# Kernel optimization log

Hardware: AMD Instinct MI355X
Metric: run time of the kernel (lower is better)

The kernel has to match this reference:

```python
import jax, jax.numpy as jnp
import numpy as np

D = 1024
H = 16
DH = D // H  # 64
B, S = 4, 1024


def setup_inputs() -> dict:
    key = jax.random.key(0)
    ks = jax.random.split(key, 7)
    sequences = jax.random.normal(ks[0], (B, S, D), dtype=jnp.float32)
    scale = 1.0 / np.sqrt(DH)
    Wq = jax.random.normal(ks[1], (H, DH, DH), dtype=jnp.float32) * scale
    Wk = jax.random.normal(ks[2], (H, DH, DH), dtype=jnp.float32) * scale
    Wv = jax.random.normal(ks[3], (H, DH, DH), dtype=jnp.float32) * scale
    bq = jax.random.normal(ks[4], (H, DH), dtype=jnp.float32) * 0.01
    bk = jax.random.normal(ks[5], (H, DH), dtype=jnp.float32) * 0.01
    bv = jax.random.normal(ks[6], (H, DH), dtype=jnp.float32) * 0.01
    return {"sequences": sequences, "Wq": Wq, "Wk": Wk, "Wv": Wv,
            "bq": bq, "bk": bk, "bv": bv}


def reference(sequences, Wq, Wk, Wv, bq, bk, bv):
    b, s, d = sequences.shape
    x = sequences.reshape(b, s, H, DH)  # split channels into heads
    # per-head Linear: y = x @ W.T + b (torch convention)
    q = jnp.einsum('bshd,hed->bshe', x, Wq) + bq
    k = jnp.einsum('bshd,hed->bshe', x, Wk) + bk
    v = jnp.einsum('bshd,hed->bshe', x, Wv) + bv
    inv_sqrt_dh = jnp.asarray(1.0 / np.sqrt(DH), dtype=sequences.dtype)
    scores = jnp.einsum('bshe,bthe->bhst', q, k) * inv_sqrt_dh  # [B,H,S,S]
    attn = jax.nn.softmax(scores, axis=-1)
    out = jnp.einsum('bhst,bthe->bshe', attn, v)  # [B,S,H,DH]
    return out.reshape(b, s, d)  # hstack of heads == reshape here
```

## Files before the change

kernel.cpp:

```cpp
#include <hip/hip_runtime.h>

#define H 16
#define DH 64
#define BB 4
#define SS 1024
#define DD 1024

typedef __attribute__((ext_vector_type(8))) short bf16x8;
typedef __attribute__((ext_vector_type(4))) float f32x4;
typedef __attribute__((ext_vector_type(4))) unsigned int u32x4;
typedef __attribute__((ext_vector_type(2))) unsigned int u32x2;
typedef _Float16 f16x4 __attribute__((ext_vector_type(4)));
typedef _Float16 f16x8 __attribute__((ext_vector_type(8)));
typedef __fp16 hf16x2 __attribute__((ext_vector_type(2)));

#define QSCALE 0.18033688011112042f

#if __has_builtin(__builtin_amdgcn_exp2f)
__device__ __forceinline__ float fast_exp2(float x) {
    return __builtin_amdgcn_exp2f(x);
}
#else
__device__ __forceinline__ float fast_exp2(float x) {
    float r;
    asm("v_exp_f32 %0, %1" : "=v"(r) : "v"(x));
    return r;
}
#endif

__device__ __forceinline__ unsigned short f2bf(float f) {
    union { float f; unsigned u; } v; v.f = f;
    unsigned u = v.u;
    return (unsigned short)((u + 0x7FFFu + ((u >> 16) & 1u)) >> 16);
}

__device__ __forceinline__ unsigned short f2h(float f) {
    union { _Float16 h; unsigned short u; } v;
    v.h = (_Float16)f;
    return v.u;
}

__device__ __forceinline__ void pack8(unsigned short* dst, f32x4 a, f32x4 b) {
    unsigned u0 = (unsigned)f2bf(a[0]) | ((unsigned)f2bf(a[1]) << 16);
    unsigned u1 = (unsigned)f2bf(a[2]) | ((unsigned)f2bf(a[3]) << 16);
    unsigned u2 = (unsigned)f2bf(b[0]) | ((unsigned)f2bf(b[1]) << 16);
    unsigned u3 = (unsigned)f2bf(b[2]) | ((unsigned)f2bf(b[3]) << 16);
    u32x4 v = {u0, u1, u2, u3};
    *(u32x4*)dst = v;
}

__device__ __forceinline__ void async_cp1k(const unsigned short* g,
                                           unsigned short* l, int lane) {
    __builtin_amdgcn_global_load_lds(
        (const __attribute__((address_space(1))) unsigned int*)(g + lane * 8),
        (__attribute__((address_space(3))) unsigned int*)l, 16, 0, 0);
}

__global__ __launch_bounds__(256) void wprep_kernel(
    const float* __restrict__ Wq, const float* __restrict__ Wk,
    const float* __restrict__ Wv, unsigned short* __restrict__ Wp)
{
    const int tg = blockIdx.x * 256 + threadIdx.x;
    const int r = tg >> 2, part = tg & 3;
    const int e = r & 63, hm = r >> 6;
    const int m = hm % 3, h = hm / 3;
    const float* src = (m == 0 ? Wq : (m == 1 ? Wk : Wv)) +
                       (size_t)(h * 64 + e) * 64 + part * 16;
    const float scale = (m == 0) ? QSCALE : 1.0f;
    f32x4 f0 = ((const f32x4*)src)[0];
    f32x4 f1 = ((const f32x4*)src)[1];
    f32x4 f2 = ((const f32x4*)src)[2];
    f32x4 f3 = ((const f32x4*)src)[3];
    f0 *= scale; f1 *= scale; f2 *= scale; f3 *= scale;
    unsigned short tmp[16];
    pack8(tmp, f0, f1);
    pack8(tmp + 8, f2, f3);
    unsigned short* dst = Wp + (size_t)(hm * 64 + e) * 64;
    const int c0 = part * 2, sw = e & 7;
    *(u32x4*)(dst + (c0 ^ sw) * 8)       = *(const u32x4*)tmp;
    *(u32x4*)(dst + ((c0 + 1) ^ sw) * 8) = *(const u32x4*)(tmp + 8);
}

__global__ __launch_bounds__(256) void qkv_kernel(
    const float* __restrict__ x, const unsigned short* __restrict__ Wp,
    const float* __restrict__ bq, const float* __restrict__ bk,
    const float* __restrict__ bv,
    unsigned short* __restrict__ Qg, unsigned short* __restrict__ Kg,
    unsigned short* __restrict__ VTg)
{
    __shared__ __align__(16) unsigned short Xl[4096];
    __shared__ __align__(16) unsigned short Wl[12288];

    const int bid = blockIdx.x;
    const int sc = bid & 15, h = (bid >> 4) & 15, b = bid >> 8;
    const int s0 = sc * 64;
    const int tid = threadIdx.x;
    const int lane = tid & 63, w = tid >> 6;

    {
        const unsigned short* wbase = Wp + (size_t)h * 12288;
#pragma unroll
        for (int sub = 0; sub < 6; sub++) {
            const int off = w * 3072 + sub * 512;
            async_cp1k(wbase + off, &Wl[off], lane);
        }
    }
    {
        const int s = tid >> 2, part = tid & 3;
        const float* src = x + ((size_t)(b * SS + s0 + s)) * DD + h * DH + part * 16;
        f32x4 f0 = ((const f32x4*)src)[0];
        f32x4 f1 = ((const f32x4*)src)[1];
        f32x4 f2 = ((const f32x4*)src)[2];
        f32x4 f3 = ((const f32x4*)src)[3];
        unsigned short tmp[16];
        pack8(tmp, f0, f1);
        pack8(tmp + 8, f2, f3);
        const int c0 = part * 2, sws = s & 7;
        *(u32x4*)&Xl[s * 64 + (c0 ^ sws) * 8]       = *(const u32x4*)tmp;
        *(u32x4*)&Xl[s * 64 + ((c0 + 1) ^ sws) * 8] = *(const u32x4*)(tmp + 8);
    }
    __syncthreads();

    const int l15 = lane & 15, quad = lane >> 4, sw = l15 & 7;

    f32x4 acc[3][4];
#pragma unroll
    for (int m = 0; m < 3; m++)
#pragma unroll
        for (int nt = 0; nt < 4; nt++) acc[m][nt] = (f32x4){0.f, 0.f, 0.f, 0.f};

#pragma unroll
    for (int k2 = 0; k2 < 2; k2++) {
        const int csw = (((k2 << 2) | quad) ^ sw) * 8;
        bf16x8 a = *(const bf16x8*)&Xl[(w * 16 + l15) * 64 + csw];
#pragma unroll
        for (int nt = 0; nt < 4; nt++) {
            const int boff = (nt * 16 + l15) * 64 + csw;
            bf16x8 b0 = *(const bf16x8*)&Wl[boff];
            acc[0][nt] = __builtin_amdgcn_mfma_f32_16x16x32_bf16(a, b0, acc[0][nt], 0, 0, 0);
            bf16x8 b1 = *(const bf16x8*)&Wl[4096 + boff];
            acc[1][nt] = __builtin_amdgcn_mfma_f32_16x16x32_bf16(a, b1, acc[1][nt], 0, 0, 0);
            bf16x8 b2 = *(const bf16x8*)&Wl[8192 + boff];
            acc[2][nt] = __builtin_amdgcn_mfma_f32_16x16x32_bf16(a, b2, acc[2][nt], 0, 0, 0);
        }
    }
    __syncthreads();

#pragma unroll
    for (int nt = 0; nt < 4; nt++) {
        const int e = nt * 16 + l15;
        const float bqs = bq[h * DH + e] * QSCALE;
        const float bks = bk[h * DH + e];
        const float bvs = bv[h * DH + e];
#pragma unroll
        for (int r = 0; r < 4; r++) {
            const int srow = w * 16 + quad * 4 + r;
            Xl[srow * 64 + e] = f2bf(acc[0][nt][r] + bqs);
            Wl[srow * 64 + e] = f2bf(acc[1][nt][r] + bks);
        }
        unsigned v01 = (unsigned)f2h(acc[2][nt][0] + bvs) |
                       ((unsigned)f2h(acc[2][nt][1] + bvs) << 16);
        unsigned v23 = (unsigned)f2h(acc[2][nt][2] + bvs) |
                       ((unsigned)f2h(acc[2][nt][3] + bvs) << 16);
        u32x2 pv = {v01, v23};
        *(u32x2*)&Wl[4096 + w * 1024 + e * 16 + quad * 4] = pv;
    }
    __syncthreads();
    {
        const size_t bh = (size_t)(b * H + h);
        const int row = tid >> 2, part = tid & 3;
        const int cg = part * 16, c0 = part * 2, swr = row & 7;
        unsigned short* qdst = Qg + (bh * SS + s0 + row) * DH + cg;
        *(u32x4*)qdst       = *(const u32x4*)&Xl[row * 64 + cg];
        *(u32x4*)(qdst + 8) = *(const u32x4*)&Xl[row * 64 + cg + 8];
        unsigned short* kbase = Kg + (bh * 16 + sc) * 4096 + row * 64;
        *(u32x4*)(kbase + (c0 ^ swr) * 8)       = *(const u32x4*)&Wl[row * 64 + c0 * 8];
        *(u32x4*)(kbase + ((c0 + 1) ^ swr) * 8) = *(const u32x4*)&Wl[row * 64 + c0 * 8 + 8];
        unsigned short* vdst = VTg + (bh * 16 + sc) * 4096 + tid * 16;
        *(u32x4*)vdst       = *(const u32x4*)&Wl[4096 + tid * 16];
        *(u32x4*)(vdst + 8) = *(const u32x4*)&Wl[4096 + tid * 16 + 8];
    }
}

__global__ __launch_bounds__(256) void attn_kernel(
    const unsigned short* __restrict__ Qg, const unsigned short* __restrict__ Kg,
    const unsigned short* __restrict__ VTg, float* __restrict__ out)
{
    __shared__ __align__(16) unsigned short L[16384];

    const int bid = blockIdx.x;
    const int bh = bid & 63, qt = bid >> 6;
    const int h = bh & 15, b = bh >> 4;
    const int tid = threadIdx.x;
    const int lane = tid & 63, w = tid >> 6;
    const int l15 = lane & 15, quad = lane >> 4, sw = l15 & 7;

    const unsigned short* Kt = Kg + (size_t)bh * 16 * 4096 + w * 1024;
    const unsigned short* Vt = VTg + (size_t)bh * 16 * 4096 + w * 1024;
    unsigned short* Lw = &L[w * 4096];

    const int kb0 = l15 * 64 + ((quad)     ^ sw) * 8;
    const int kb1 = l15 * 64 + ((4 | quad) ^ sw) * 8;
    const int vb  = 1024 + l15 * 16 + quad * 4;

    bf16x8 aQ0[4], aQ1[4];
#pragma unroll
    for (int qb = 0; qb < 4; qb++) {
        const unsigned short* qp =
            Qg + ((size_t)bh * SS + qt * 64 + qb * 16 + l15) * DH + quad * 8;
        aQ0[qb] = *(const bf16x8*)(qp);
        aQ1[qb] = *(const bf16x8*)(qp + 32);
    }

    auto stage = [&](int kt, int bufb) {
        const unsigned short* kg = Kt + kt * 4096;
        const unsigned short* vg = Vt + kt * 4096;
        unsigned short* lb = Lw + bufb * 2048;
        async_cp1k(kg,       lb,        lane);
        async_cp1k(kg + 512, lb + 512,  lane);
        async_cp1k(vg,       lb + 1024, lane);
        async_cp1k(vg + 512, lb + 1536, lane);
    };

    stage(0, 0);
    stage(1, 1);

    f32x4 accO[4][4];
#pragma unroll
    for (int et = 0; et < 4; et++)
#pragma unroll
        for (int qb = 0; qb < 4; qb++) accO[et][qb] = (f32x4){0.f, 0.f, 0.f, 0.f};
    float rs[4] = {0.f, 0.f, 0.f, 0.f};

#pragma unroll
    for (int kt = 0; kt < 16; kt++) {
        if (kt < 15) asm volatile("s_waitcnt vmcnt(4)" ::: "memory");
        else         asm volatile("s_waitcnt vmcnt(0)" ::: "memory");
        const unsigned short* Bc = Lw + (kt & 1) * 2048;

        bf16x8 aK0 = *(const bf16x8*)(Bc + kb0);
        bf16x8 aK1 = *(const bf16x8*)(Bc + kb1);
        f16x4 aV[4];
#pragma unroll
        for (int et = 0; et < 4; et++)
            aV[et] = *(const f16x4*)(Bc + vb + et * 256);
        asm volatile("s_waitcnt lgkmcnt(0)" ::: "memory");
        if (kt < 14) stage(kt + 2, kt & 1);

        f32x4 sc[4];
#pragma unroll
        for (int qb = 0; qb < 4; qb++) {
            f32x4 z = {0.f, 0.f, 0.f, 0.f};
            z = __builtin_amdgcn_mfma_f32_16x16x32_bf16(aK0, aQ0[qb], z, 0, 0, 0);
            z = __builtin_amdgcn_mfma_f32_16x16x32_bf16(aK1, aQ1[qb], z, 0, 0, 0);
            sc[qb] = z;
        }

        f16x4 pf[4];
#pragma unroll
        for (int qb = 0; qb < 4; qb++) {
            float p0 = fast_exp2(sc[qb][0]);
            float p1 = fast_exp2(sc[qb][1]);
            float p2 = fast_exp2(sc[qb][2]);
            float p3 = fast_exp2(sc[qb][3]);
            rs[qb] += (p0 + p1) + (p2 + p3);
            union { hf16x2 h; unsigned u; } lo, hi;
            lo.h = __builtin_amdgcn_cvt_pkrtz(p0, p1);
            hi.h = __builtin_amdgcn_cvt_pkrtz(p2, p3);
            union { unsigned u[2]; f16x4 v; } pk;
            pk.u[0] = lo.u; pk.u[1] = hi.u;
            pf[qb] = pk.v;
        }

#pragma unroll
        for (int et = 0; et < 4; et++) {
#pragma unroll
            for (int qb = 0; qb < 4; qb++)
                accO[et][qb] = __builtin_amdgcn_mfma_f32_16x16x16f16(
                    aV[et], pf[qb], accO[et][qb], 0, 0, 0);
        }
    }

#pragma unroll
    for (int qb = 0; qb < 4; qb++) {
        rs[qb] += __shfl_xor(rs[qb], 16);
        rs[qb] += __shfl_xor(rs[qb], 32);
    }

    __syncthreads();

    float* R  = (float*)L;
    float* R2 = (float*)L + 5120;
    if (quad == 0) {
#pragma unroll
        for (int qb = 0; qb < 4; qb++) R2[w * 64 + qb * 16 + l15] = rs[qb];
    }

    const int q = tid >> 2, eg = tid & 3;
    float inv = 0.f;
#pragma unroll
    for (int et = 0; et < 4; et++) {
#pragma unroll
        for (int qb = 0; qb < 4; qb++)
            *(f32x4*)&R[w * 1280 + (qb * 16 + l15) * 20 + quad * 4] = accO[et][qb];
        __syncthreads();
        if (et == 0)
            inv = 1.0f / (R2[q] + R2[64 + q] + R2[128 + q] + R2[192 + q]);
        f32x4 o0 = *(const f32x4*)&R[q * 20 + eg * 4];
        f32x4 o1 = *(const f32x4*)&R[1280 + q * 20 + eg * 4];
        f32x4 o2 = *(const f32x4*)&R[2560 + q * 20 + eg * 4];
        f32x4 o3 = *(const f32x4*)&R[3840 + q * 20 + eg * 4];
        f32x4 o = ((o0 + o1) + (o2 + o3)) * inv;
        float* op = out + ((size_t)b * SS + qt * 64 + q) * DD + h * DH + et * 16 + eg * 4;
        *(f32x4*)op = o;
        if (et < 3) __syncthreads();
    }
}

extern "C" void kernel_launch(void* const* d_in, const int* in_sizes, int n_in,
                              void* d_out, int out_size, void* d_ws, size_t ws_size,
                              hipStream_t stream) {
    const float* x  = (const float*)d_in[0];
    const float* Wq = (const float*)d_in[1];
    const float* Wk = (const float*)d_in[2];
    const float* Wv = (const float*)d_in[3];
    const float* bq = (const float*)d_in[4];
    const float* bk = (const float*)d_in[5];
    const float* bv = (const float*)d_in[6];

    const size_t NE = (size_t)BB * H * SS * DH;
    unsigned short* Qg  = (unsigned short*)d_ws;
    unsigned short* Kg  = Qg + NE;
    unsigned short* VTg = Kg + NE;
    unsigned short* Wp  = VTg + NE;

    wprep_kernel<<<48, 256, 0, stream>>>(Wq, Wk, Wv, Wp);
    qkv_kernel<<<BB * H * (SS / 64), 256, 0, stream>>>(x, Wp, bq, bk, bv,
                                                       Qg, Kg, VTg);
    attn_kernel<<<BB * H * 16, 256, 0, stream>>>(Qg, Kg, VTg, (float*)d_out);
}
```

Baseline: 116.9 us.

## Fuse weight prep into QKV kernel and stage Q through LDS in attention

Removes the separate weight-prep kernel launch. Each QKV block now converts, scales and swizzles its head's fp32 weights into LDS directly, which repeats that conversion per block. Q is written in the same swizzled tile layout as K. The attention kernel loads Q into LDS asynchronously and reads the fragments per key tile instead of holding them in registers, with a 4-blocks-per-CU launch bound to cut register pressure and raise occupancy. In exchange it adds LDS reads per tile and more LDS use per block.

```diff
diff --git a/kernel.cpp b/kernel.cpp
--- a/kernel.cpp
+++ b/kernel.cpp
@@ -56,33 +56,10 @@
         (__attribute__((address_space(3))) unsigned int*)l, 16, 0, 0);
 }
 
-__global__ __launch_bounds__(256) void wprep_kernel(
+__global__ __launch_bounds__(256) void qkv_kernel(
+    const float* __restrict__ x,
     const float* __restrict__ Wq, const float* __restrict__ Wk,
-    const float* __restrict__ Wv, unsigned short* __restrict__ Wp)
-{
-    const int tg = blockIdx.x * 256 + threadIdx.x;
-    const int r = tg >> 2, part = tg & 3;
-    const int e = r & 63, hm = r >> 6;
-    const int m = hm % 3, h = hm / 3;
-    const float* src = (m == 0 ? Wq : (m == 1 ? Wk : Wv)) +
-                       (size_t)(h * 64 + e) * 64 + part * 16;
-    const float scale = (m == 0) ? QSCALE : 1.0f;
-    f32x4 f0 = ((const f32x4*)src)[0];
-    f32x4 f1 = ((const f32x4*)src)[1];
-    f32x4 f2 = ((const f32x4*)src)[2];
-    f32x4 f3 = ((const f32x4*)src)[3];
-    f0 *= scale; f1 *= scale; f2 *= scale; f3 *= scale;
-    unsigned short tmp[16];
-    pack8(tmp, f0, f1);
-    pack8(tmp + 8, f2, f3);
-    unsigned short* dst = Wp + (size_t)(hm * 64 + e) * 64;
-    const int c0 = part * 2, sw = e & 7;
-    *(u32x4*)(dst + (c0 ^ sw) * 8)       = *(const u32x4*)tmp;
-    *(u32x4*)(dst + ((c0 + 1) ^ sw) * 8) = *(const u32x4*)(tmp + 8);
-}
-
-__global__ __launch_bounds__(256) void qkv_kernel(
-    const float* __restrict__ x, const unsigned short* __restrict__ Wp,
+    const float* __restrict__ Wv,
     const float* __restrict__ bq, const float* __restrict__ bk,
     const float* __restrict__ bv,
     unsigned short* __restrict__ Qg, unsigned short* __restrict__ Kg,
@@ -97,13 +74,26 @@
     const int tid = threadIdx.x;
     const int lane = tid & 63, w = tid >> 6;
 
-    {
-        const unsigned short* wbase = Wp + (size_t)h * 12288;
-#pragma unroll
-        for (int sub = 0; sub < 6; sub++) {
-            const int off = w * 3072 + sub * 512;
-            async_cp1k(wbase + off, &Wl[off], lane);
-        }
+#pragma unroll
+    for (int i = 0; i < 3; i++) {
+        const int task = tid + i * 256;
+        const int r = task >> 2, part = task & 3;
+        const int m = r >> 6, e = r & 63;
+        const float* src = (m == 0 ? Wq : (m == 1 ? Wk : Wv)) +
+                           (size_t)(h * 64 + e) * 64 + part * 16;
+        const float scale = (m == 0) ? QSCALE : 1.0f;
+        f32x4 f0 = ((const f32x4*)src)[0];
+        f32x4 f1 = ((const f32x4*)src)[1];
+        f32x4 f2 = ((const f32x4*)src)[2];
+        f32x4 f3 = ((const f32x4*)src)[3];
+        f0 *= scale; f1 *= scale; f2 *= scale; f3 *= scale;
+        unsigned short tmp[16];
+        pack8(tmp, f0, f1);
+        pack8(tmp + 8, f2, f3);
+        unsigned short* dst = &Wl[m * 4096 + e * 64];
+        const int c0 = part * 2, swe = e & 7;
+        *(u32x4*)(dst + (c0 ^ swe) * 8)       = *(const u32x4*)tmp;
+        *(u32x4*)(dst + ((c0 + 1) ^ swe) * 8) = *(const u32x4*)(tmp + 8);
     }
     {
         const int s = tid >> 2, part = tid & 3;
@@ -169,10 +159,10 @@
     {
         const size_t bh = (size_t)(b * H + h);
         const int row = tid >> 2, part = tid & 3;
-        const int cg = part * 16, c0 = part * 2, swr = row & 7;
-        unsigned short* qdst = Qg + (bh * SS + s0 + row) * DH + cg;
-        *(u32x4*)qdst       = *(const u32x4*)&Xl[row * 64 + cg];
-        *(u32x4*)(qdst + 8) = *(const u32x4*)&Xl[row * 64 + cg + 8];
+        const int c0 = part * 2, swr = row & 7;
+        unsigned short* qbase = Qg + (bh * 16 + sc) * 4096 + row * 64;
+        *(u32x4*)(qbase + (c0 ^ swr) * 8)       = *(const u32x4*)&Xl[row * 64 + c0 * 8];
+        *(u32x4*)(qbase + ((c0 + 1) ^ swr) * 8) = *(const u32x4*)&Xl[row * 64 + c0 * 8 + 8];
         unsigned short* kbase = Kg + (bh * 16 + sc) * 4096 + row * 64;
         *(u32x4*)(kbase + (c0 ^ swr) * 8)       = *(const u32x4*)&Wl[row * 64 + c0 * 8];
         *(u32x4*)(kbase + ((c0 + 1) ^ swr) * 8) = *(const u32x4*)&Wl[row * 64 + c0 * 8 + 8];
@@ -182,11 +172,12 @@
     }
 }
 
-__global__ __launch_bounds__(256) void attn_kernel(
+__global__ __launch_bounds__(256, 4) void attn_kernel(
     const unsigned short* __restrict__ Qg, const unsigned short* __restrict__ Kg,
     const unsigned short* __restrict__ VTg, float* __restrict__ out)
 {
     __shared__ __align__(16) unsigned short L[16384];
+    __shared__ __align__(16) unsigned short Ql[4096];
 
     const int bid = blockIdx.x;
     const int bh = bid & 63, qt = bid >> 6;
@@ -197,20 +188,16 @@
 
     const unsigned short* Kt = Kg + (size_t)bh * 16 * 4096 + w * 1024;
     const unsigned short* Vt = VTg + (size_t)bh * 16 * 4096 + w * 1024;
+    const unsigned short* Qt = Qg + ((size_t)bh * 16 + qt) * 4096;
     unsigned short* Lw = &L[w * 4096];
 
     const int kb0 = l15 * 64 + ((quad)     ^ sw) * 8;
     const int kb1 = l15 * 64 + ((4 | quad) ^ sw) * 8;
     const int vb  = 1024 + l15 * 16 + quad * 4;
 
-    bf16x8 aQ0[4], aQ1[4];
-#pragma unroll
-    for (int qb = 0; qb < 4; qb++) {
-        const unsigned short* qp =
-            Qg + ((size_t)bh * SS + qt * 64 + qb * 16 + l15) * DH + quad * 8;
-        aQ0[qb] = *(const bf16x8*)(qp);
-        aQ1[qb] = *(const bf16x8*)(qp + 32);
-    }
+    async_cp1k(Qt + w * 1024,       Ql + w * 1024,       lane);
+    async_cp1k(Qt + w * 1024 + 512, Ql + w * 1024 + 512, lane);
+    __syncthreads();
 
     auto stage = [&](int kt, int bufb) {
         const unsigned short* kg = Kt + kt * 4096;
@@ -250,9 +237,11 @@
         f32x4 sc[4];
 #pragma unroll
         for (int qb = 0; qb < 4; qb++) {
+            bf16x8 aQ0 = *(const bf16x8*)(Ql + kb0 + qb * 1024);
+            bf16x8 aQ1 = *(const bf16x8*)(Ql + kb1 + qb * 1024);
             f32x4 z = {0.f, 0.f, 0.f, 0.f};
-            z = __builtin_amdgcn_mfma_f32_16x16x32_bf16(aK0, aQ0[qb], z, 0, 0, 0);
-            z = __builtin_amdgcn_mfma_f32_16x16x32_bf16(aK1, aQ1[qb], z, 0, 0, 0);
+            z = __builtin_amdgcn_mfma_f32_16x16x32_bf16(aK0, aQ0, z, 0, 0, 0);
+            z = __builtin_amdgcn_mfma_f32_16x16x32_bf16(aK1, aQ1, z, 0, 0, 0);
             sc[qb] = z;
         }
 
@@ -332,10 +321,8 @@
     unsigned short* Qg  = (unsigned short*)d_ws;
     unsigned short* Kg  = Qg + NE;
     unsigned short* VTg = Kg + NE;
-    unsigned short* Wp  = VTg + NE;
-
-    wprep_kernel<<<48, 256, 0, stream>>>(Wq, Wk, Wv, Wp);
-    qkv_kernel<<<BB * H * (SS / 64), 256, 0, stream>>>(x, Wp, bq, bk, bv,
-                                                       Qg, Kg, VTg);
+
+    qkv_kernel<<<BB * H * (SS / 64), 256, 0, stream>>>(x, Wq, Wk, Wv,
+                                                       bq, bk, bv, Qg, Kg, VTg);
     attn_kernel<<<BB * H * 16, 256, 0, stream>>>(Qg, Kg, VTg, (float*)d_out);
 }
```

After: 117.9 us. Within noise of the previous version (+0.8%).
